# Optimization experiments

Measured on AMD Instinct MI355X. Metric: run time of the kernel, lower is better.

Reference implementation:

```python
import jax, jax.numpy as jnp
import numpy as np

AGENT_TYPE_VEHICLE = 1
AGENT_TYPE_PEDESTRIAN = 2
N_VEHICLE_INTENTIONS = 6
N_PEDESTRIAN_INTENTIONS = 2
INTENTION_LOGIT_DIM = 6


def setup_inputs() -> dict:
    key = jax.random.key(0)
    ks = jax.random.split(key, 10)
    B, N, D = 32, 2048, 512
    H = D // 2
    s_in = 1.0 / np.sqrt(D)
    s_h = 1.0 / np.sqrt(H)
    return {
        "repr3": jax.random.normal(ks[0], (B, N, D), dtype=jnp.float32),
        "agent_type_ids": jax.random.randint(ks[1], (B, N), 0, 4, dtype=jnp.int64),
        # vehicle head: Linear(D, D//2) -> GELU -> Linear(D//2, 6)
        "vW1": jax.random.normal(ks[2], (H, D), dtype=jnp.float32) * s_in,
        "vb1": jax.random.normal(ks[3], (H,), dtype=jnp.float32) * s_in,
        "vW2": jax.random.normal(ks[4], (N_VEHICLE_INTENTIONS, H), dtype=jnp.float32) * s_h,
        "vb2": jax.random.normal(ks[5], (N_VEHICLE_INTENTIONS,), dtype=jnp.float32) * s_h,
        # pedestrian head: Linear(D, D//2) -> GELU -> Linear(D//2, 2)
        "pW1": jax.random.normal(ks[6], (H, D), dtype=jnp.float32) * s_in,
        "pb1": jax.random.normal(ks[7], (H,), dtype=jnp.float32) * s_in,
        "pW2": jax.random.normal(ks[8], (N_PEDESTRIAN_INTENTIONS, H), dtype=jnp.float32) * s_h,
        "pb2": jax.random.normal(ks[9], (N_PEDESTRIAN_INTENTIONS,), dtype=jnp.float32) * s_h,
    }


def _mlp(x, W1, b1, W2, b2):
    # x: [B,N,D] -> [B,N,out]; exact (erf) GELU matches torch nn.GELU()
    h = jax.nn.gelu(jnp.einsum("bnd,hd->bnh", x, W1) + b1, approximate=False)
    return jnp.einsum("bnh,oh->bno", h, W2) + b2


def reference(repr3, agent_type_ids, vW1, vb1, vW2, vb2, pW1, pb1, pW2, pb2):
    v_mask = agent_type_ids == AGENT_TYPE_VEHICLE  # [B,N]
    p_mask = agent_type_ids == AGENT_TYPE_PEDESTRIAN
    v_logits = _mlp(repr3, vW1, vb1, vW2, vb2)  # [B,N,6]
    p_logits = _mlp(repr3, pW1, pb1, pW2, pb2)  # [B,N,2]
    pad = INTENTION_LOGIT_DIM - N_PEDESTRIAN_INTENTIONS
    p_padded = jnp.pad(p_logits, ((0, 0), (0, 0), (0, pad)))  # [B,N,6]
    zero = jnp.zeros((), dtype=repr3.dtype)
    intention_logits = (
        jnp.where(v_mask[..., None], v_logits, zero)
        + jnp.where(p_mask[..., None], p_padded, zero)
    )
    return intention_logits, v_mask, p_mask
```

## Files before the change

### kernel.cpp

```cpp
#include <hip/hip_runtime.h>
#include <hip/hip_bf16.h>
#include <math.h>


#define TOKENS 65536
#define DIM    512
#define HID    256
#define ASTR   40
#define ABUFB  5120
#define HSTR   264

using short8 = __attribute__((ext_vector_type(8))) short;
using f32x4  = __attribute__((ext_vector_type(4))) float;

#define BAR()                                                      \
    do {                                                           \
        __builtin_amdgcn_sched_barrier(0);                         \
        asm volatile("s_waitcnt lgkmcnt(0)" ::: "memory");         \
        __builtin_amdgcn_s_barrier();                              \
        __builtin_amdgcn_sched_barrier(0);                         \
    } while (0)

__device__ __forceinline__ unsigned int pkrne(float a, float b) {
    unsigned int ua = __float_as_uint(a);
    unsigned int ub = __float_as_uint(b);
    ua += 0x7FFFu + ((ua >> 16) & 1u);
    ub += 0x7FFFu + ((ub >> 16) & 1u);
    return __builtin_amdgcn_perm(ub, ua, 0x07060302u);
}

__device__ __forceinline__ uint2 cvt4(f32x4 v) {
    return make_uint2(pkrne(v[0], v[1]), pkrne(v[2], v[3]));
}

__device__ __forceinline__ __hip_bfloat16 bf16rne(float x) {
    unsigned int u = __float_as_uint(x);
    u += 0x7FFFu + ((u >> 16) & 1u);
    unsigned short hs = (unsigned short)(u >> 16);
    return *(__hip_bfloat16*)&hs;
}

__device__ __forceinline__ float gelu_exact(float x) {
    const float z  = fabsf(x) * 0.7071067811865475f;
    const float t  = __builtin_amdgcn_rcpf(fmaf(0.3275911f, z, 1.0f));
    float p = fmaf(1.061405429f, t, -1.453152027f);
    p = fmaf(p, t, 1.421413741f);
    p = fmaf(p, t, -0.284496736f);
    p = fmaf(p, t, 0.254829592f);
    p = p * t;
    const float e  = __expf(-z * z);
    const float er = fmaf(-p, e, 1.0f);
    return 0.5f * x * (1.0f + copysignf(er, x));
}

__global__ __launch_bounds__(256)
void prep_kernel(const float* __restrict__ vW1, const float* __restrict__ pW1,
                 const float* __restrict__ vW2, const float* __restrict__ pW2,
                 __hip_bfloat16* __restrict__ Wc, __hip_bfloat16* __restrict__ W2c)
{
    const int i = blockIdx.x * 256 + threadIdx.x;
    if (i < 32768) {
        const int lane = i & 63;
        const int it   = (i >> 6) & 15;
        const int nt   = i >> 10;
        const int head = nt >> 4;
        const int row  = (nt & 15) * 16 + (lane & 15);
        const int k    = it * 32 + (lane >> 4) * 8;
        const float* src = (head ? pW1 : vW1) + row * DIM + k;
        f32x4 a = *(const f32x4*)(src);
        f32x4 b = *(const f32x4*)(src + 4);
        uint2 lo = cvt4(a), hi = cvt4(b);
        *(uint4*)((char*)Wc + (long)i * 16) = make_uint4(lo.x, lo.y, hi.x, hi.y);
    } else if (i < 32768 + 1024) {
        const int c    = i - 32768;
        const int lane = c & 63;
        const int rest = c >> 6;
        const int head = rest & 1;
        const int ks   = rest >> 1;
        const int l16  = lane & 15;
        const int quad = lane >> 4;
        const int nOut = head ? 2 : 6;
        uint4 o = make_uint4(0u, 0u, 0u, 0u);
        if (l16 < nOut) {
            const float* src = (head ? pW2 : vW2) + l16 * HID + ks * 32 + quad * 8;
            f32x4 a = *(const f32x4*)(src);
            f32x4 b = *(const f32x4*)(src + 4);
            uint2 lo = cvt4(a), hi = cvt4(b);
            o = make_uint4(lo.x, lo.y, hi.x, hi.y);
        }
        *(uint4*)((char*)W2c + (long)c * 16) = o;
    }
}

__global__ __launch_bounds__(256, 4)
void intention_heads_kernel(const float* __restrict__ X,
                            const int* __restrict__ ids,
                            const __hip_bfloat16* __restrict__ Wc,
                            const __hip_bfloat16* __restrict__ W2c,
                            const float* __restrict__ vb1,
                            const float* __restrict__ pb1,
                            const float* __restrict__ vb2,
                            const float* __restrict__ pb2,
                            float* __restrict__ out)
{
    __shared__ __align__(16) unsigned char smem[64 * HSTR * 2];
    __hip_bfloat16* H = (__hip_bfloat16*)smem;

    const int cpx = gridDim.x >> 3;
    const int bid = (blockIdx.x & 7) * cpx + (blockIdx.x >> 3);

    const int head = bid & 1;
    const int row0 = (bid >> 1) * 64;

    const int tid  = threadIdx.x;
    const int wave = tid >> 6;
    const int lane = tid & 63;
    const int quad = lane >> 4;
    const int l16  = lane & 15;
    const int wcol = wave * 64;

    const int q  = tid & 7;
    const int r2 = tid >> 3;
    const float* Xs = X + (long)(row0 + r2) * DIM + q * 4;

    const char* Bq = (const char*)Wc
                   + (long)(head * 16 + wave * 4) * 16384 + (long)lane * 16;

    f32x4 acc[4][4];
    #pragma unroll
    for (int i = 0; i < 4; ++i)
        #pragma unroll
        for (int j = 0; j < 4; ++j)
            acc[i][j] = (f32x4){0.f, 0.f, 0.f, 0.f};

    f32x4 ga0 = *(const f32x4*)(Xs);
    f32x4 ga1 = *(const f32x4*)(Xs + 32 * DIM);
    f32x4 gb0 = *(const f32x4*)(Xs + 32);
    f32x4 gb1 = *(const f32x4*)(Xs + 32 * DIM + 32);
    {
        __hip_bfloat16* A = (__hip_bfloat16*)smem;
        *(uint2*)&A[r2 * ASTR + q * 4]        = cvt4(ga0);
        *(uint2*)&A[(r2 + 32) * ASTR + q * 4] = cvt4(ga1);
    }
    BAR();
    ga0 = gb0; ga1 = gb1;

    #pragma unroll
    for (int it = 0; it < DIM / 32; ++it) {
        __hip_bfloat16* cur = (__hip_bfloat16*)(smem + (it % 3) * ABUFB);
        __hip_bfloat16* nxt = (__hip_bfloat16*)(smem + ((it + 1) % 3) * ABUFB);

        if (it < 14) {
            gb0 = *(const f32x4*)(Xs + (it + 2) * 32);
            gb1 = *(const f32x4*)(Xs + 32 * DIM + (it + 2) * 32);
        }

        short8 bc[4];
        #pragma unroll
        for (int j = 0; j < 4; ++j)
            bc[j] = *(const short8*)(Bq + j * 16384 + it * 1024);

        short8 af[4];
        #pragma unroll
        for (int i = 0; i < 4; ++i)
            af[i] = *(const short8*)&cur[(i * 16 + l16) * ASTR + quad * 8];

        #pragma unroll
        for (int i = 0; i < 4; ++i)
            #pragma unroll
            for (int j = 0; j < 4; ++j)
                acc[i][j] = __builtin_amdgcn_mfma_f32_16x16x32_bf16(af[i], bc[j], acc[i][j], 0, 0, 0);

        if (it < 15) {
            *(uint2*)&nxt[r2 * ASTR + q * 4]        = cvt4(ga0);
            *(uint2*)&nxt[(r2 + 32) * ASTR + q * 4] = cvt4(ga1);
        }
        BAR();
        ga0 = gb0; ga1 = gb1;
    }

    const float* b1 = head ? pb1 : vb1;
    float b1v[4];
    #pragma unroll
    for (int j = 0; j < 4; ++j)
        b1v[j] = b1[wcol + j * 16 + l16];

    #pragma unroll
    for (int i = 0; i < 4; ++i) {
        #pragma unroll
        for (int j = 0; j < 4; ++j) {
            const int col = wcol + j * 16 + l16;
            #pragma unroll
            for (int rr = 0; rr < 4; ++rr) {
                const int row = i * 16 + quad * 4 + rr;
                H[row * HSTR + col] = bf16rne(gelu_exact(acc[i][j][rr] + b1v[j]));
            }
        }
    }
    BAR();

    const float* b2 = head ? pb2 : vb2;
    const int nOut = head ? 2 : 6;

    f32x4 acc2 = (f32x4){0.f, 0.f, 0.f, 0.f};
    const int tokb = wave * 16;
    const short* hbase = (const short*)&H[(tokb + l16) * HSTR + quad * 8];
    const char*  w2q   = (const char*)W2c + head * 1024 + (long)lane * 16;
    #pragma unroll
    for (int ks = 0; ks < 8; ++ks) {
        short8 af    = *(const short8*)(hbase + ks * 32);
        short8 bfrag = *(const short8*)(w2q + ks * 2048);
        acc2 = __builtin_amdgcn_mfma_f32_16x16x32_bf16(af, bfrag, acc2, 0, 0, 0);
    }

    const float b2v = (l16 < nOut) ? b2[l16] : 0.0f;

    #pragma unroll
    for (int rr = 0; rr < 4; ++rr) {
        const int t = row0 + tokb + quad * 4 + rr;
        const int type = ids[t];
        if (head == 0) {
            if (l16 == 0) {
                out[TOKENS * 6 + t] = (type == 1) ? 1.0f : 0.0f;
                out[TOKENS * 7 + t] = (type == 2) ? 1.0f : 0.0f;
            }
            if (l16 < 6) {
                if (type == 1)
                    out[t * 6 + l16] = acc2[rr] + b2v;
                else if (type != 2)
                    out[t * 6 + l16] = 0.0f;
            }
        } else {
            if (l16 < 6 && type == 2)
                out[t * 6 + l16] = (l16 < 2) ? (acc2[rr] + b2v) : 0.0f;
        }
    }
}

extern "C" void kernel_launch(void* const* d_in, const int* in_sizes, int n_in,
                              void* d_out, int out_size, void* d_ws, size_t ws_size,
                              hipStream_t stream) {
    (void)n_in; (void)out_size; (void)ws_size;
    const float* X   = (const float*)d_in[0];
    const int*   ids = (const int*)d_in[1];
    const float* vW1 = (const float*)d_in[2];
    const float* vb1 = (const float*)d_in[3];
    const float* vW2 = (const float*)d_in[4];
    const float* vb2 = (const float*)d_in[5];
    const float* pW1 = (const float*)d_in[6];
    const float* pb1 = (const float*)d_in[7];
    const float* pW2 = (const float*)d_in[8];
    const float* pb2 = (const float*)d_in[9];
    float* out = (float*)d_out;

    __hip_bfloat16* Wc  = (__hip_bfloat16*)d_ws;
    __hip_bfloat16* W2c = Wc + 512 * DIM;

    hipLaunchKernelGGL(prep_kernel, dim3(132), dim3(256), 0, stream,
                       vW1, pW1, vW2, pW2, Wc, W2c);

    const int tokens = in_sizes[1];
    const int grid   = (tokens / 64) * 2;

    hipLaunchKernelGGL(intention_heads_kernel, dim3(grid), dim3(256), 0, stream,
                       X, ids, Wc, W2c, vb1, pb1, vb2, pb2, out);
}
```

Measured before the change: 272.5 us.

## Double block size to 8 waves, halve per-wave tile, use double-buffered A

Each block now runs 512 threads (8 waves). Every wave computes a 64x32 slice of the hidden layer instead of 64x64, which halves its accumulator registers and raises the occupancy target. The X staging buffer drops from triple to double buffering with a one-step prefetch, since each thread now loads one row. The second-layer matmul and the output stores run only on the first four waves. The change trades shallower prefetch and more waves per barrier for more latency hiding through occupancy.

```diff
diff --git a/kernel.cpp b/kernel.cpp
--- a/kernel.cpp
+++ b/kernel.cpp
@@ -7,7 +7,6 @@
 #define DIM    512
 #define HID    256
 #define ASTR   40
-#define ABUFB  5120
 #define HSTR   264
 
 using short8 = __attribute__((ext_vector_type(8))) short;
@@ -92,7 +91,7 @@
     }
 }
 
-__global__ __launch_bounds__(256, 4)
+__global__ __launch_bounds__(512, 6)
 void intention_heads_kernel(const float* __restrict__ X,
                             const int* __restrict__ ids,
                             const __hip_bfloat16* __restrict__ Wc,
@@ -117,47 +116,40 @@
     const int lane = tid & 63;
     const int quad = lane >> 4;
     const int l16  = lane & 15;
-    const int wcol = wave * 64;
-
-    const int q  = tid & 7;
-    const int r2 = tid >> 3;
-    const float* Xs = X + (long)(row0 + r2) * DIM + q * 4;
+    const int wcol = wave * 32;
+
+    const int q = tid & 7;
+    const int r = tid >> 3;
+    const float* Xs = X + (long)(row0 + r) * DIM + q * 4;
 
     const char* Bq = (const char*)Wc
-                   + (long)(head * 16 + wave * 4) * 16384 + (long)lane * 16;
-
-    f32x4 acc[4][4];
+                   + (long)(head * 16 + wave * 2) * 16384 + (long)lane * 16;
+
+    f32x4 acc[4][2];
     #pragma unroll
     for (int i = 0; i < 4; ++i)
         #pragma unroll
-        for (int j = 0; j < 4; ++j)
+        for (int j = 0; j < 2; ++j)
             acc[i][j] = (f32x4){0.f, 0.f, 0.f, 0.f};
 
-    f32x4 ga0 = *(const f32x4*)(Xs);
-    f32x4 ga1 = *(const f32x4*)(Xs + 32 * DIM);
-    f32x4 gb0 = *(const f32x4*)(Xs + 32);
-    f32x4 gb1 = *(const f32x4*)(Xs + 32 * DIM + 32);
+    f32x4 ga = *(const f32x4*)(Xs);
     {
         __hip_bfloat16* A = (__hip_bfloat16*)smem;
-        *(uint2*)&A[r2 * ASTR + q * 4]        = cvt4(ga0);
-        *(uint2*)&A[(r2 + 32) * ASTR + q * 4] = cvt4(ga1);
+        *(uint2*)&A[r * ASTR + q * 4] = cvt4(ga);
     }
     BAR();
-    ga0 = gb0; ga1 = gb1;
 
     #pragma unroll
     for (int it = 0; it < DIM / 32; ++it) {
-        __hip_bfloat16* cur = (__hip_bfloat16*)(smem + (it % 3) * ABUFB);
-        __hip_bfloat16* nxt = (__hip_bfloat16*)(smem + ((it + 1) % 3) * ABUFB);
-
-        if (it < 14) {
-            gb0 = *(const f32x4*)(Xs + (it + 2) * 32);
-            gb1 = *(const f32x4*)(Xs + 32 * DIM + (it + 2) * 32);
-        }
-
-        short8 bc[4];
-        #pragma unroll
-        for (int j = 0; j < 4; ++j)
+        __hip_bfloat16* cur = (__hip_bfloat16*)(smem + (it & 1) * 5120);
+        __hip_bfloat16* nxt = (__hip_bfloat16*)(smem + ((it + 1) & 1) * 5120);
+
+        if (it < 15)
+            ga = *(const f32x4*)(Xs + (it + 1) * 32);
+
+        short8 bc[2];
+        #pragma unroll
+        for (int j = 0; j < 2; ++j)
             bc[j] = *(const short8*)(Bq + j * 16384 + it * 1024);
 
         short8 af[4];
@@ -168,27 +160,24 @@
         #pragma unroll
         for (int i = 0; i < 4; ++i)
             #pragma unroll
-            for (int j = 0; j < 4; ++j)
+            for (int j = 0; j < 2; ++j)
                 acc[i][j] = __builtin_amdgcn_mfma_f32_16x16x32_bf16(af[i], bc[j], acc[i][j], 0, 0, 0);
 
-        if (it < 15) {
-            *(uint2*)&nxt[r2 * ASTR + q * 4]        = cvt4(ga0);
-            *(uint2*)&nxt[(r2 + 32) * ASTR + q * 4] = cvt4(ga1);
-        }
+        if (it < 15)
+            *(uint2*)&nxt[r * ASTR + q * 4] = cvt4(ga);
         BAR();
-        ga0 = gb0; ga1 = gb1;
     }
 
     const float* b1 = head ? pb1 : vb1;
-    float b1v[4];
-    #pragma unroll
-    for (int j = 0; j < 4; ++j)
+    float b1v[2];
+    #pragma unroll
+    for (int j = 0; j < 2; ++j)
         b1v[j] = b1[wcol + j * 16 + l16];
 
     #pragma unroll
     for (int i = 0; i < 4; ++i) {
         #pragma unroll
-        for (int j = 0; j < 4; ++j) {
+        for (int j = 0; j < 2; ++j) {
             const int col = wcol + j * 16 + l16;
             #pragma unroll
             for (int rr = 0; rr < 4; ++rr) {
@@ -199,40 +188,42 @@
     }
     BAR();
 
-    const float* b2 = head ? pb2 : vb2;
-    const int nOut = head ? 2 : 6;
-
-    f32x4 acc2 = (f32x4){0.f, 0.f, 0.f, 0.f};
-    const int tokb = wave * 16;
-    const short* hbase = (const short*)&H[(tokb + l16) * HSTR + quad * 8];
-    const char*  w2q   = (const char*)W2c + head * 1024 + (long)lane * 16;
-    #pragma unroll
-    for (int ks = 0; ks < 8; ++ks) {
-        short8 af    = *(const short8*)(hbase + ks * 32);
-        short8 bfrag = *(const short8*)(w2q + ks * 2048);
-        acc2 = __builtin_amdgcn_mfma_f32_16x16x32_bf16(af, bfrag, acc2, 0, 0, 0);
-    }
-
-    const float b2v = (l16 < nOut) ? b2[l16] : 0.0f;
-
-    #pragma unroll
-    for (int rr = 0; rr < 4; ++rr) {
-        const int t = row0 + tokb + quad * 4 + rr;
-        const int type = ids[t];
-        if (head == 0) {
-            if (l16 == 0) {
-                out[TOKENS * 6 + t] = (type == 1) ? 1.0f : 0.0f;
-                out[TOKENS * 7 + t] = (type == 2) ? 1.0f : 0.0f;
+    if (wave < 4) {
+        const float* b2 = head ? pb2 : vb2;
+        const int nOut = head ? 2 : 6;
+
+        f32x4 acc2 = (f32x4){0.f, 0.f, 0.f, 0.f};
+        const int tokb = wave * 16;
+        const short* hbase = (const short*)&H[(tokb + l16) * HSTR + quad * 8];
+        const char*  w2q   = (const char*)W2c + head * 1024 + (long)lane * 16;
+        #pragma unroll
+        for (int ks = 0; ks < 8; ++ks) {
+            short8 af    = *(const short8*)(hbase + ks * 32);
+            short8 bfrag = *(const short8*)(w2q + ks * 2048);
+            acc2 = __builtin_amdgcn_mfma_f32_16x16x32_bf16(af, bfrag, acc2, 0, 0, 0);
+        }
+
+        const float b2v = (l16 < nOut) ? b2[l16] : 0.0f;
+
+        #pragma unroll
+        for (int rr = 0; rr < 4; ++rr) {
+            const int t = row0 + tokb + quad * 4 + rr;
+            const int type = ids[t];
+            if (head == 0) {
+                if (l16 == 0) {
+                    out[TOKENS * 6 + t] = (type == 1) ? 1.0f : 0.0f;
+                    out[TOKENS * 7 + t] = (type == 2) ? 1.0f : 0.0f;
+                }
+                if (l16 < 6) {
+                    if (type == 1)
+                        out[t * 6 + l16] = acc2[rr] + b2v;
+                    else if (type != 2)
+                        out[t * 6 + l16] = 0.0f;
+                }
+            } else {
+                if (l16 < 6 && type == 2)
+                    out[t * 6 + l16] = (l16 < 2) ? (acc2[rr] + b2v) : 0.0f;
             }
-            if (l16 < 6) {
-                if (type == 1)
-                    out[t * 6 + l16] = acc2[rr] + b2v;
-                else if (type != 2)
-                    out[t * 6 + l16] = 0.0f;
-            }
-        } else {
-            if (l16 < 6 && type == 2)
-                out[t * 6 + l16] = (l16 < 2) ? (acc2[rr] + b2v) : 0.0f;
         }
     }
 }
@@ -262,6 +253,6 @@
     const int tokens = in_sizes[1];
     const int grid   = (tokens / 64) * 2;
 
-    hipLaunchKernelGGL(intention_heads_kernel, dim3(grid), dim3(256), 0, stream,
+    hipLaunchKernelGGL(intention_heads_kernel, dim3(grid), dim3(512), 0, stream,
                        X, ids, Wc, W2c, vb1, pb1, vb2, pb2, out);
 }
```

New measurement: 253.9 us. 6.8% less time.
